# Performance work log

Measured on AMD Instinct MI355X. Metric: run time of the kernel, lower is better.

The kernel has to match this reference:

```python
import jax, jax.numpy as jnp
import numpy as np

IN_DIM = 256
HID = 384
HEADS = 6
NH1 = HID // HEADS  # 64 per-head hidden in layer1
N = 3072
SLOPE_GAT = 0.2   # LeakyReLU inside GAT attention
SLOPE_ACT = 0.01  # default nn.LeakyReLU / F.leaky_relu slope


def _leaky(x, s):
    return jnp.where(x >= 0, x, s * x)


def _gat_sublayer(h, mask, W, a, heads, nh, concat):
    # h: [N, F_in], mask: [N, N] bool, W: [heads*nh, F_in], a: [2*nh]
    n = h.shape[0]
    g = (h @ W.T).reshape(n, heads, nh)  # [N, H, F]
    # e[i,j,h] = leakyrelu(<g_i, a_l> + <g_j, a_r>)  (avoids O(N^2) concat)
    sl = jnp.einsum('nhf,f->nh', g, a[:nh])
    sr = jnp.einsum('nhf,f->nh', g, a[nh:])
    e = _leaky(sl[:, None, :] + sr[None, :, :], SLOPE_GAT)  # [N, N, H]
    e = jnp.where(mask[:, :, None], e, jnp.float32(-10000.0))
    att = jax.nn.softmax(e, axis=1)  # softmax over source nodes j
    out = jnp.einsum('ijh,jhf->ihf', att, g)
    return out.reshape(n, heads * nh) if concat else out.mean(axis=1)


def _gat(x, mask, W1, a1, W2, a2):
    x = _gat_sublayer(x, mask, W1, a1, HEADS, NH1, True)   # [N, HID]
    x = jax.nn.elu(x)
    return _gat_sublayer(x, mask, W2, a2, 1, IN_DIM, False)  # [N, IN_DIM]


def setup_inputs() -> dict:
    key = jax.random.key(0)
    ks = iter(jax.random.split(key, 32))
    d = {
        'feature': jax.random.normal(next(ks), (1, N, IN_DIM), jnp.float32),
        'adj': jax.random.randint(next(ks), (1, N, N), 0, 2, jnp.int32),
        'doc_num': 16,
        'sect_num': 192,
    }
    def w(shape, scale=0.05):
        return jax.random.normal(next(ks), shape, jnp.float32) * scale
    for br in ('sent', 'sect', 'doc'):
        d[f'W1_{br}'] = w((HID, IN_DIM))
        d[f'a1_{br}'] = w((2 * NH1,))
        d[f'W2_{br}'] = w((IN_DIM, HID))
        d[f'a2_{br}'] = w((2 * IN_DIM,))
    d['fusion_W'] = w((IN_DIM, 3 * IN_DIM)); d['fusion_b'] = jnp.zeros((IN_DIM,), jnp.float32)
    d['ffn_W0'] = w((HID, IN_DIM)); d['ffn_b0'] = jnp.zeros((HID,), jnp.float32)
    d['ffn_W1'] = w((HID, HID)); d['ffn_b1'] = jnp.zeros((HID,), jnp.float32)
    d['ffn_W2'] = w((IN_DIM, HID)); d['ffn_b2'] = jnp.zeros((IN_DIM,), jnp.float32)
    return d


def reference(feature, adj, doc_num, sect_num,
              W1_sent, a1_sent, W2_sent, a2_sent,
              W1_sect, a1_sect, W2_sect, a2_sect,
              W1_doc, a1_doc, W2_doc, a2_doc,
              fusion_W, fusion_b,
              ffn_W0, ffn_b0, ffn_W1, ffn_b1, ffn_W2, ffn_b2):
    f = feature[0]          # [N, D]
    n = f.shape[0]
    A = adj[0] != 0         # [N, N]
    cols = jnp.arange(n)
    sent_mask = A & (cols < n - sect_num - doc_num)[None, :]
    sect_mask = A & (cols >= n - sect_num - doc_num)[None, :] & (cols < n - doc_num)[None, :]
    doc_mask = A & (cols >= n - doc_num)[None, :]

    f_sent = _gat(f, sent_mask, W1_sent, a1_sent, W2_sent, a2_sent) + f
    f_sect = _gat(f, sect_mask, W1_sect, a1_sect, W2_sect, a2_sect) + f
    f_doc = _gat(f, doc_mask, W1_doc, a1_doc, W2_doc, a2_doc) + f

    fused = jnp.concatenate([f_doc, f_sect, f_sent], axis=-1)  # [N, 3D]
    fused = _leaky(fused @ fusion_W.T + fusion_b, SLOPE_ACT)
    h = _leaky(fused @ ffn_W0.T + ffn_b0, SLOPE_ACT)
    h = _leaky(h @ ffn_W1.T + ffn_b1, SLOPE_ACT)
    h = _leaky(h @ ffn_W2.T + ffn_b2, SLOPE_ACT)
    return (h + f)[None]    # [1, N, D]
```

## Files before the change

kernel.cpp:

```cpp
#include <hip/hip_runtime.h>
#include <stdint.h>

#define N_NODES 3072
#define D_IN    256
#define HIDDEN  384
#define HEADS   6
#define NH1     64
#define C1      1152
#define C2      768
#define MASK_ULL   48
#define MASK_BYTES 384
#define MASK_BSTRIDE ((size_t)N_NODES * MASK_BYTES)
#define QS      6
#define LOG2E   1.4426950408889634f

typedef __bf16 bf16;
typedef __bf16 bf16x8 __attribute__((ext_vector_type(8)));
typedef __bf16 bf16x4 __attribute__((ext_vector_type(4)));
typedef float  f32x4  __attribute__((ext_vector_type(4)));

__device__ __forceinline__ void atomAddF(float* p, float v) {
  __hip_atomic_fetch_add(p, v, __ATOMIC_RELAXED, __HIP_MEMORY_SCOPE_AGENT);
}
__device__ __forceinline__ float fexp2(float x) {
  float r; asm("v_exp_f32 %0, %1" : "=v"(r) : "v"(x)); return r;
}
__device__ __forceinline__ int bnd32(int jlo, int jhi, int len, int q, int Qb) {
  return (q >= Qb) ? ((jhi + 31) & ~31) : ((jlo + (len * q) / Qb) & ~31);
}

struct CastArgs {
  const float* src[11];
  bf16*        dst[11];
  int          cum4[12];
  int          castN;
};

__global__ __launch_bounds__(256) void prep_kernel(CastArgs A,
                                                   const int* __restrict__ adj,
                                                   unsigned long long* __restrict__ maskU,
                                                   const int* __restrict__ dnum,
                                                   const int* __restrict__ snum) {
  if ((int)blockIdx.x < A.castN) {
    int g = blockIdx.x * 256 + threadIdx.x;
    int j = 0;
#pragma unroll
    for (int k = 1; k < 11; ++k) j += (g >= A.cum4[k]);
    int e = (g - A.cum4[j]) * 4;
    float4 v = *(const float4*)(A.src[j] + e);
    bf16x4 o = { (bf16)v.x, (bf16)v.y, (bf16)v.z, (bf16)v.w };
    *(bf16x4*)(A.dst[j] + e) = o;
    return;
  }
  int dn = dnum[0], sn = snum[0];
  int bb1 = N_NODES - sn - dn, bb2 = N_NODES - dn;
  int row = blockIdx.x - A.castN;
  const int* ar = adj + (size_t)row * N_NODES;
  int lane = threadIdx.x & 63, wave = threadIdx.x >> 6;
#pragma unroll
  for (int it = 0; it < N_NODES / 256; ++it) {
    int j = it * 256 + wave * 64 + lane;
    bool a = ar[j] != 0;
    unsigned long long m0 = __ballot(a && (j < bb1));
    unsigned long long m1 = __ballot(a && (j >= bb1) && (j < bb2));
    unsigned long long m2 = __ballot(a && (j >= bb2));
    if (lane == 0) {
      size_t o = (size_t)row * MASK_ULL + it * 4 + wave;
      maskU[o] = m0;
      maskU[o + (size_t)N_NODES * MASK_ULL] = m1;
      maskU[o + 2 * (size_t)N_NODES * MASK_ULL] = m2;
    }
  }
}

template<int C>
__global__ __launch_bounds__(256) void pack_kernel(const bf16* __restrict__ src,
                                                   bf16* __restrict__ dst,
                                                   float* __restrict__ gm) {
  __shared__ bf16 t[64][72];
  int j0 = blockIdx.x * 64, f0 = blockIdx.y * 64;
  int rr = threadIdx.x >> 4;
  int cc = (threadIdx.x & 15) * 4;
#pragma unroll
  for (int p = 0; p < 4; ++p) {
    int r = p * 16 + rr;
    *(bf16x4*)&t[r][cc] = *(const bf16x4*)&src[(size_t)(j0 + r) * C + f0 + cc];
  }
  __syncthreads();
  int f = threadIdx.x & 63, g = threadIdx.x >> 6;
#pragma unroll
  for (int q = 0; q < 2; ++q) {
    int p = g * 2 + q;
    bf16x8 v = { t[p*8+0][f], t[p*8+1][f], t[p*8+2][f], t[p*8+3][f],
                 t[p*8+4][f], t[p*8+5][f], t[p*8+6][f], t[p*8+7][f] };
    *(bf16x8*)&dst[ ((size_t)((j0 >> 3) + p) * C + f0 + f) * 8 ] = v;
  }
  float s = 0.f;
#pragma unroll
  for (int k = 0; k < 16; ++k) s += (float)t[g * 16 + k][f];
  atomAddF(&gm[f0 + f], s * (1.0f / N_NODES));
}

template<int NCPB, int NH>
__global__ __launch_bounds__(256) void head_proj_kernel(
    const bf16* __restrict__ g, int ldg,
    const float* __restrict__ a0, const float* __restrict__ a1, const float* __restrict__ a2,
    float* __restrict__ elp, float* __restrict__ eln,
    float* __restrict__ erp, float* __restrict__ ern) {
  int c = blockIdx.y;
  int i = blockIdx.x * 16 + (threadIdx.x >> 4);
  int b = c / NCPB;
  const float* a = (b == 0) ? a0 : (b == 1) ? a1 : a2;
  int f0 = (threadIdx.x & 15) * (NH / 16);
  const bf16* gr = g + (size_t)i * ldg + c * NH + f0;
  float accl = 0.f, accr = 0.f;
#pragma unroll
  for (int k = 0; k < NH / 16; k += 4) {
    bf16x4 v = *(const bf16x4*)&gr[k];
#pragma unroll
    for (int e = 0; e < 4; ++e) {
      float gv = (float)v[e];
      accl += gv * a[f0 + k + e];
      accr += gv * a[NH + f0 + k + e];
    }
  }
#pragma unroll
  for (int m = 1; m < 16; m <<= 1) {
    accl += __shfl_xor(accl, m, 64);
    accr += __shfl_xor(accr, m, 64);
  }
  if ((threadIdx.x & 15) == 0) {
    int o = c * N_NODES + i;
    elp[o] = fexp2(accl * LOG2E);
    eln[o] = fexp2(0.2f * accl * LOG2E);
    erp[o] = fexp2(accr * LOG2E);
    ern[o] = fexp2(0.2f * accr * LOG2E);
  }
}

template<bool BIAS, bool LEAKY, bool RES, bool F32OUT>
__global__ __launch_bounds__(256) void gemm64_kernel(
    const bf16* __restrict__ A, int lda, int aZoff,
    const bf16* __restrict__ B0, const bf16* __restrict__ B1, const bf16* __restrict__ B2,
    int ldb, void* __restrict__ Cout, int ldc, int cZoff, int K,
    const float* __restrict__ bias, const float* __restrict__ res) {
  __shared__ bf16 As[2 * 64 * 64];
  __shared__ bf16 Bs[2 * 64 * 64];
  int z = blockIdx.z;
  const bf16* Ab = A + (size_t)z * aZoff;
  const bf16* Bb = (z == 0) ? B0 : (z == 1) ? B1 : B2;
  int m0 = blockIdx.x * 64, n0 = blockIdx.y * 64;
  int tid = threadIdx.x;
  int lane = tid & 63, wave = tid >> 6;
  int wm = wave >> 1, wn = wave & 1;
  int l15 = lane & 15, lk = lane >> 4;
  int r0 = tid >> 3, p0 = tid & 7, q0 = p0 ^ (r0 & 7);
  int r1 = (256 + tid) >> 3, p1 = tid & 7, q1 = p1 ^ (r1 & 7);
  bf16x8 ra0, ra1, rb0, rb1;
  auto gload = [&](int kt) {
    const bf16* ab = Ab + (size_t)kt * 64;
    const bf16* bb = Bb + (size_t)kt * 64;
    ra0 = *(const bf16x8*)&ab[(size_t)(m0 + r0) * lda + q0 * 8];
    ra1 = *(const bf16x8*)&ab[(size_t)(m0 + r1) * lda + q1 * 8];
    rb0 = *(const bf16x8*)&bb[(size_t)(n0 + r0) * ldb + q0 * 8];
    rb1 = *(const bf16x8*)&bb[(size_t)(n0 + r1) * ldb + q1 * 8];
  };
  auto sstore = [&](int buf) {
    bf16* as = As + buf * 4096;
    bf16* bs = Bs + buf * 4096;
    *(bf16x8*)&as[r0 * 64 + p0 * 8] = ra0;
    *(bf16x8*)&as[r1 * 64 + p1 * 8] = ra1;
    *(bf16x8*)&bs[r0 * 64 + p0 * 8] = rb0;
    *(bf16x8*)&bs[r1 * 64 + p1 * 8] = rb1;
  };
  f32x4 acc[2][2] = {};
  int nk = K >> 6;
  gload(0);
  sstore(0);
  __syncthreads();
  for (int kt = 0; kt < nk; ++kt) {
    bool more = (kt + 1) < nk;
    if (more) gload(kt + 1);
    const bf16* as = As + (kt & 1) * 4096;
    const bf16* bs = Bs + (kt & 1) * 4096;
#pragma unroll
    for (int s = 0; s < 2; ++s) {
      bf16x8 af[2], bfr[2];
      int u = s * 4 + lk;
#pragma unroll
      for (int mi = 0; mi < 2; ++mi) {
        int r = wm * 32 + mi * 16 + l15;
        af[mi] = *(const bf16x8*)&as[r * 64 + (u ^ (r & 7)) * 8];
      }
#pragma unroll
      for (int ni = 0; ni < 2; ++ni) {
        int r = wn * 32 + ni * 16 + l15;
        bfr[ni] = *(const bf16x8*)&bs[r * 64 + (u ^ (r & 7)) * 8];
      }
#pragma unroll
      for (int mi = 0; mi < 2; ++mi)
#pragma unroll
        for (int ni = 0; ni < 2; ++ni)
          acc[mi][ni] = __builtin_amdgcn_mfma_f32_16x16x32_bf16(af[mi], bfr[ni], acc[mi][ni], 0, 0, 0);
    }
    if (more) sstore((kt + 1) & 1);
    __syncthreads();
  }
#pragma unroll
  for (int mi = 0; mi < 2; ++mi)
#pragma unroll
    for (int ni = 0; ni < 2; ++ni)
#pragma unroll
      for (int r = 0; r < 4; ++r) {
        int i = m0 + wm * 32 + mi * 16 + lk * 4 + r;
        int col = z * cZoff + n0 + wn * 32 + ni * 16 + l15;
        float v = acc[mi][ni][r];
        if (BIAS) v += bias[col];
        if (LEAKY) v = (v >= 0.f) ? v : 0.01f * v;
        if (RES) v += res[(size_t)i * ldc + col];
        if (F32OUT) ((float*)Cout)[(size_t)i * ldc + col] = v;
        else        ((bf16*)Cout)[(size_t)i * ldc + col] = (bf16)v;
      }
}

struct Stream {
  float4 p0, p1, n0, n1;
  unsigned int m0, m1, m2, m3;
  bf16x8 b0, b1, b2, b3;
};

template<int C>
__device__ __forceinline__ void load_stream(
    Stream& s, int jb,
    const float* __restrict__ erpB, const float* __restrict__ ernB,
    const unsigned char* mr0, const unsigned char* mr1,
    const unsigned char* mr2, const unsigned char* mr3,
    const bf16* __restrict__ gPl) {
  s.p0 = *(const float4*)&erpB[jb];
  s.p1 = *(const float4*)&erpB[jb + 4];
  s.n0 = *(const float4*)&ernB[jb];
  s.n1 = *(const float4*)&ernB[jb + 4];
  int mo = jb >> 3;
  s.m0 = mr0[mo]; s.m1 = mr1[mo]; s.m2 = mr2[mo]; s.m3 = mr3[mo];
  const bf16* gp = gPl + (size_t)mo * C * 8;
  s.b0 = *(const bf16x8*)(gp + 0);
  s.b1 = *(const bf16x8*)(gp + 128);
  s.b2 = *(const bf16x8*)(gp + 256);
  s.b3 = *(const bf16x8*)(gp + 384);
}

template<bool L1>
__global__ __launch_bounds__(256, 2) void att_kernel(
    const bf16* __restrict__ gP,
    const float* __restrict__ elpA, const float* __restrict__ elnA,
    const float* __restrict__ erpA, const float* __restrict__ ernA,
    const unsigned char* __restrict__ maskB,
    const int* __restrict__ dnum, const int* __restrict__ snum,
    float* __restrict__ accP, float* __restrict__ lP) {
  constexpr int C = L1 ? C1 : C2;
  int c = blockIdx.y;
  int b = L1 ? (c / 6) : (c >> 2);
  int colbase = L1 ? c * 64 : (b * 256 + (c & 3) * 64);
  int sidx = L1 ? c : b;
  int q = blockIdx.z;
  int Qb = (b == 0) ? QS : 1;
  if (q >= Qb) return;
  int dn = dnum[0], sn = snum[0];
  int bb1 = N_NODES - sn - dn, bb2 = N_NODES - dn;
  int jlo = (b == 0) ? 0 : (b == 1) ? bb1 : bb2;
  int jhi = (b == 0) ? bb1 : (b == 1) ? bb2 : N_NODES;
  int len = jhi - jlo;
  int wlo = bnd32(jlo, jhi, len, q, Qb);
  int whi = bnd32(jlo, jhi, len, q + 1, Qb);
  if (wlo >= whi) return;

  int wave = threadIdx.x >> 6, lane = threadIdx.x & 63;
  int l15 = lane & 15, lk = lane >> 4;
  int row0 = blockIdx.x * 256 + wave * 64;
  float elp[4], eln[4];
  const unsigned char* mr0;
  const unsigned char* mr1;
  const unsigned char* mr2;
  const unsigned char* mr3;
  {
    const unsigned char* mbase = maskB + (size_t)b * MASK_BSTRIDE;
#pragma unroll
    for (int rg = 0; rg < 4; ++rg) {
      int ip = row0 + rg * 16 + l15;
      elp[rg] = elpA[sidx * N_NODES + ip];
      eln[rg] = elnA[sidx * N_NODES + ip];
    }
    mr0 = mbase + (size_t)(row0 + 0 * 16 + l15) * MASK_BYTES;
    mr1 = mbase + (size_t)(row0 + 1 * 16 + l15) * MASK_BYTES;
    mr2 = mbase + (size_t)(row0 + 2 * 16 + l15) * MASK_BYTES;
    mr3 = mbase + (size_t)(row0 + 3 * 16 + l15) * MASK_BYTES;
  }
  const float* erpB = erpA + sidx * N_NODES;
  const float* ernB = ernA + sidx * N_NODES;
  const bf16* gPl = gP + (size_t)(colbase + l15) * 8;
  bf16x8 ones;
#pragma unroll
  for (int e = 0; e < 8; ++e) ones[e] = (bf16)1.0f;
  f32x4 acc[4][4] = {};
  f32x4 accl[4] = {};

  auto compute = [&](const Stream& cur) {
    float pv[8] = { cur.p0.x, cur.p0.y, cur.p0.z, cur.p0.w, cur.p1.x, cur.p1.y, cur.p1.z, cur.p1.w };
    float nv[8] = { cur.n0.x, cur.n0.y, cur.n0.z, cur.n0.w, cur.n1.x, cur.n1.y, cur.n1.z, cur.n1.w };
#pragma unroll
    for (int rg = 0; rg < 4; ++rg) {
      unsigned int mb = (rg == 0) ? cur.m0 : (rg == 1) ? cur.m1 : (rg == 2) ? cur.m2 : cur.m3;
      bf16x8 a8;
#pragma unroll
      for (int e = 0; e < 8; ++e) {
        float z = elp[rg] * pv[e];
        float w = eln[rg] * nv[e];
        float p = (z >= 1.f) ? z : w;
        p = ((mb >> e) & 1u) ? p : 0.f;
        a8[e] = (bf16)p;
      }
      acc[rg][0] = __builtin_amdgcn_mfma_f32_16x16x32_bf16(a8, cur.b0, acc[rg][0], 0, 0, 0);
      acc[rg][1] = __builtin_amdgcn_mfma_f32_16x16x32_bf16(a8, cur.b1, acc[rg][1], 0, 0, 0);
      acc[rg][2] = __builtin_amdgcn_mfma_f32_16x16x32_bf16(a8, cur.b2, acc[rg][2], 0, 0, 0);
      acc[rg][3] = __builtin_amdgcn_mfma_f32_16x16x32_bf16(a8, cur.b3, acc[rg][3], 0, 0, 0);
      accl[rg] = __builtin_amdgcn_mfma_f32_16x16x32_bf16(a8, ones, accl[rg], 0, 0, 0);
    }
  };

  Stream s0, s1;
  load_stream<C>(s0, wlo + lk * 8, erpB, ernB, mr0, mr1, mr2, mr3, gPl);
  int jt = wlo;
  while (true) {
    bool m1 = (jt + 32) < whi;
    if (m1) load_stream<C>(s1, jt + 32 + lk * 8, erpB, ernB, mr0, mr1, mr2, mr3, gPl);
    compute(s0);
    if (!m1) break;
    bool m2 = (jt + 64) < whi;
    if (m2) load_stream<C>(s0, jt + 64 + lk * 8, erpB, ernB, mr0, mr1, mr2, mr3, gPl);
    compute(s1);
    if (!m2) break;
    jt += 64;
  }

  int slot = (b == 0) ? (c * QS + q) : (L1 ? (36 + (c - 6)) : (24 + (c - 4)));
  float* ap = accP + ((size_t)slot * N_NODES + row0) * 64;
#pragma unroll
  for (int rg = 0; rg < 4; ++rg)
#pragma unroll
    for (int nf = 0; nf < 4; ++nf)
#pragma unroll
      for (int r = 0; r < 4; ++r)
        ap[(rg * 16 + lk * 4 + r) * 64 + nf * 16 + l15] = acc[rg][nf][r];
  if (l15 == 0) {
#pragma unroll
    for (int rg = 0; rg < 4; ++rg)
#pragma unroll
      for (int r = 0; r < 4; ++r)
        lP[(size_t)slot * N_NODES + row0 + rg * 16 + lk * 4 + r] = accl[rg][r];
  }
}

__global__ __launch_bounds__(256) void fin1_kernel(
    const float* __restrict__ accP, const float* __restrict__ lP,
    const float* __restrict__ gm, const int* __restrict__ dnum, const int* __restrict__ snum,
    bf16* __restrict__ out1) {
  int t = blockIdx.x * 256 + threadIdx.x;
  int i = t / (C1 / 8), f0 = (t - i * (C1 / 8)) * 8;
  int c = f0 >> 6;
  int b = c / 6;
  int dn = dnum[0], sn = snum[0];
  int bb1 = N_NODES - sn - dn, bb2 = N_NODES - dn;
  int jlo = (b == 0) ? 0 : (b == 1) ? bb1 : bb2;
  int jhi = (b == 0) ? bb1 : (b == 1) ? bb2 : N_NODES;
  int len = jhi - jlo;
  int Qb = (b == 0) ? QS : 1;
  float l = 0.f;
  float a[8] = {0.f,0.f,0.f,0.f,0.f,0.f,0.f,0.f};
  if (len > 0) {
    for (int q = 0; q < Qb; ++q) {
      if (bnd32(jlo, jhi, len, q, Qb) >= bnd32(jlo, jhi, len, q + 1, Qb)) continue;
      int slot = (b == 0) ? (c * QS + q) : (36 + (c - 6));
      l += lP[(size_t)slot * N_NODES + i];
      const float* ap = &accP[((size_t)slot * N_NODES + i) * 64 + (f0 & 63)];
      f32x4 v0 = *(const f32x4*)ap, v1 = *(const f32x4*)(ap + 4);
#pragma unroll
      for (int e = 0; e < 4; ++e) { a[e] += v0[e]; a[e + 4] += v1[e]; }
    }
  }
  float inv = (l > 0.f) ? 1.f / l : 0.f;
  bf16x8 o;
#pragma unroll
  for (int e = 0; e < 8; ++e) {
    float v = (l > 0.f) ? a[e] * inv : gm[f0 + e];
    v = (v > 0.f) ? v : (__expf(v) - 1.f);
    o[e] = (bf16)v;
  }
  *(bf16x8*)&out1[(size_t)i * C1 + f0] = o;
}

__global__ __launch_bounds__(256) void fin2_kernel(
    const float* __restrict__ accP, const float* __restrict__ lP,
    const float* __restrict__ gm, const float* __restrict__ feat,
    const int* __restrict__ dnum, const int* __restrict__ snum,
    bf16* __restrict__ fused) {
  int t = blockIdx.x * 256 + threadIdx.x;
  int i = t / (C2 / 8), f0 = (t - i * (C2 / 8)) * 8;
  int b = f0 >> 8;
  int fi = f0 & 255;
  int fc = (f0 >> 6) & 3;
  int c = b * 4 + fc;
  int dn = dnum[0], sn = snum[0];
  int bb1 = N_NODES - sn - dn, bb2 = N_NODES - dn;
  int jlo = (b == 0) ? 0 : (b == 1) ? bb1 : bb2;
  int jhi = (b == 0) ? bb1 : (b == 1) ? bb2 : N_NODES;
  int len = jhi - jlo;
  int Qb = (b == 0) ? QS : 1;
  float l = 0.f;
  float a[8] = {0.f,0.f,0.f,0.f,0.f,0.f,0.f,0.f};
  if (len > 0) {
    for (int q = 0; q < Qb; ++q) {
      if (bnd32(jlo, jhi, len, q, Qb) >= bnd32(jlo, jhi, len, q + 1, Qb)) continue;
      int slot = (b == 0) ? (c * QS + q) : (24 + (c - 4));
      l += lP[(size_t)slot * N_NODES + i];
      const float* ap = &accP[((size_t)slot * N_NODES + i) * 64 + (f0 & 63)];
      f32x4 v0 = *(const f32x4*)ap, v1 = *(const f32x4*)(ap + 4);
#pragma unroll
      for (int e = 0; e < 4; ++e) { a[e] += v0[e]; a[e + 4] += v1[e]; }
    }
  }
  float inv = (l > 0.f) ? 1.f / l : 0.f;
  bf16x8 o;
#pragma unroll
  for (int e = 0; e < 8; ++e) {
    float v = (l > 0.f) ? a[e] * inv : gm[f0 + e];
    v += feat[(size_t)i * D_IN + fi + e];
    o[e] = (bf16)v;
  }
  *(bf16x8*)&fused[(size_t)i * C2 + (2 - b) * D_IN + fi] = o;
}

extern "C" void kernel_launch(void* const* d_in, const int* in_sizes, int n_in,
                              void* d_out, int out_size, void* d_ws, size_t ws_size,
                              hipStream_t stream) {
  (void)in_sizes; (void)n_in; (void)out_size; (void)ws_size;
  const float* feature = (const float*)d_in[0];
  const int*   adj     = (const int*)d_in[1];
  const int*   dnum    = (const int*)d_in[2];
  const int*   snum    = (const int*)d_in[3];
  const float* W1s = (const float*)d_in[4];  const float* a1s = (const float*)d_in[5];
  const float* W2s = (const float*)d_in[6];  const float* a2s = (const float*)d_in[7];
  const float* W1e = (const float*)d_in[8];  const float* a1e = (const float*)d_in[9];
  const float* W2e = (const float*)d_in[10]; const float* a2e = (const float*)d_in[11];
  const float* W1d = (const float*)d_in[12]; const float* a1d = (const float*)d_in[13];
  const float* W2d = (const float*)d_in[14]; const float* a2d = (const float*)d_in[15];
  const float* fW  = (const float*)d_in[16]; const float* fB  = (const float*)d_in[17];
  const float* w0  = (const float*)d_in[18]; const float* b0  = (const float*)d_in[19];
  const float* w1  = (const float*)d_in[20]; const float* b1  = (const float*)d_in[21];
  const float* w2  = (const float*)d_in[22]; const float* b2  = (const float*)d_in[23];

  char* ws = (char*)d_ws;
  size_t off = 0;
  auto alloc = [&](size_t bytes) { void* p = ws + off; off += (bytes + 255) & ~(size_t)255; return p; };

  unsigned long long* maskU = (unsigned long long*)alloc(3 * (size_t)N_NODES * MASK_ULL * 8);
  bf16* fbf   = (bf16*)alloc((size_t)N_NODES * D_IN * 2);
  bf16* w1b0  = (bf16*)alloc(HIDDEN * D_IN * 2);
  bf16* w1b1  = (bf16*)alloc(HIDDEN * D_IN * 2);
  bf16* w1b2  = (bf16*)alloc(HIDDEN * D_IN * 2);
  bf16* w2b0  = (bf16*)alloc(D_IN * HIDDEN * 2);
  bf16* w2b1  = (bf16*)alloc(D_IN * HIDDEN * 2);
  bf16* w2b2  = (bf16*)alloc(D_IN * HIDDEN * 2);
  bf16* wfusb = (bf16*)alloc(D_IN * C2 * 2);
  bf16* wf0b  = (bf16*)alloc(HIDDEN * D_IN * 2);
  bf16* wf1b  = (bf16*)alloc(HIDDEN * HIDDEN * 2);
  bf16* wf2b  = (bf16*)alloc(D_IN * HIDDEN * 2);
  bf16* g1    = (bf16*)alloc((size_t)N_NODES * C1 * 2);
  bf16* gP1   = (bf16*)alloc((size_t)N_NODES * C1 * 2);
  bf16* out1  = (bf16*)alloc((size_t)N_NODES * C1 * 2);
  bf16* g2    = (bf16*)alloc((size_t)N_NODES * C2 * 2);
  bf16* gP2   = (bf16*)alloc((size_t)N_NODES * C2 * 2);
  bf16* fusedB= (bf16*)alloc((size_t)N_NODES * C2 * 2);
  bf16* h0    = (bf16*)alloc((size_t)N_NODES * D_IN * 2);
  bf16* h1    = (bf16*)alloc((size_t)N_NODES * HIDDEN * 2);
  bf16* h2    = (bf16*)alloc((size_t)N_NODES * HIDDEN * 2);
  float* elp1 = (float*)alloc(18 * N_NODES * 4);
  float* eln1 = (float*)alloc(18 * N_NODES * 4);
  float* erp1 = (float*)alloc(18 * N_NODES * 4);
  float* ern1 = (float*)alloc(18 * N_NODES * 4);
  float* elp2 = (float*)alloc(3 * N_NODES * 4);
  float* eln2 = (float*)alloc(3 * N_NODES * 4);
  float* erp2 = (float*)alloc(3 * N_NODES * 4);
  float* ern2 = (float*)alloc(3 * N_NODES * 4);
  float* accU = (float*)alloc((size_t)48 * N_NODES * 64 * 4);
  float* lU   = (float*)alloc((size_t)48 * N_NODES * 4);
  size_t zoff = off;
  float* gm1  = (float*)alloc(C1 * 4);
  float* gm2  = (float*)alloc(C2 * 4);
  size_t zbytes = off - zoff;
  const unsigned char* maskBytes = (const unsigned char*)maskU;

  hipMemsetAsync(ws + zoff, 0, zbytes, stream);

  CastArgs ca;
  {
    const float* srcs[11] = { feature, W1s, W1e, W1d, W2s, W2e, W2d, fW, w0, w1, w2 };
    bf16* dsts[11] = { fbf, w1b0, w1b1, w1b2, w2b0, w2b1, w2b2, wfusb, wf0b, wf1b, wf2b };
    int counts[11] = { N_NODES*D_IN, HIDDEN*D_IN, HIDDEN*D_IN, HIDDEN*D_IN,
                       D_IN*HIDDEN, D_IN*HIDDEN, D_IN*HIDDEN, D_IN*C2,
                       HIDDEN*D_IN, HIDDEN*HIDDEN, D_IN*HIDDEN };
    int cum = 0;
    for (int k = 0; k < 11; ++k) { ca.src[k] = srcs[k]; ca.dst[k] = dsts[k]; ca.cum4[k] = cum; cum += counts[k] / 4; }
    ca.cum4[11] = cum;
    ca.castN = cum / 256;
    prep_kernel<<<ca.castN + N_NODES, 256, 0, stream>>>(ca, adj, maskU, dnum, snum);
  }
  gemm64_kernel<false,false,false,false><<<dim3(48,6,3), 256, 0, stream>>>(
      fbf, D_IN, 0, w1b0, w1b1, w1b2, D_IN, g1, C1, HIDDEN, D_IN, nullptr, nullptr);
  pack_kernel<C1><<<dim3(48,18), 256, 0, stream>>>(g1, gP1, gm1);
  head_proj_kernel<HEADS, NH1><<<dim3(192,18), 256, 0, stream>>>(g1, C1, a1s, a1e, a1d, elp1, eln1, erp1, ern1);
  att_kernel<true><<<dim3(12, 18, QS), 256, 0, stream>>>(gP1, elp1, eln1, erp1, ern1, maskBytes, dnum, snum, accU, lU);
  fin1_kernel<<<N_NODES * (C1 / 8) / 256, 256, 0, stream>>>(accU, lU, gm1, dnum, snum, out1);
  gemm64_kernel<false,false,false,false><<<dim3(48,4,3), 256, 0, stream>>>(
      out1, C1, HIDDEN, w2b0, w2b1, w2b2, HIDDEN, g2, C2, D_IN, HIDDEN, nullptr, nullptr);
  pack_kernel<C2><<<dim3(48,12), 256, 0, stream>>>(g2, gP2, gm2);
  head_proj_kernel<1, D_IN><<<dim3(192,3), 256, 0, stream>>>(g2, C2, a2s, a2e, a2d, elp2, eln2, erp2, ern2);
  att_kernel<false><<<dim3(12, 12, QS), 256, 0, stream>>>(gP2, elp2, eln2, erp2, ern2, maskBytes, dnum, snum, accU, lU);
  fin2_kernel<<<N_NODES * (C2 / 8) / 256, 256, 0, stream>>>(accU, lU, gm2, feature, dnum, snum, fusedB);
  gemm64_kernel<true,true,false,false><<<dim3(48,4,1), 256, 0, stream>>>(
      fusedB, C2, 0, wfusb, wfusb, wfusb, C2, h0, D_IN, 0, C2, fB, nullptr);
  gemm64_kernel<true,true,false,false><<<dim3(48,6,1), 256, 0, stream>>>(
      h0, D_IN, 0, wf0b, wf0b, wf0b, D_IN, h1, HIDDEN, 0, D_IN, b0, nullptr);
  gemm64_kernel<true,true,false,false><<<dim3(48,6,1), 256, 0, stream>>>(
      h1, HIDDEN, 0, wf1b, wf1b, wf1b, HIDDEN, h2, HIDDEN, 0, HIDDEN, b1, nullptr);
  gemm64_kernel<true,true,true,true><<<dim3(48,4,1), 256, 0, stream>>>(
      h2, HIDDEN, 0, wf2b, wf2b, wf2b, HIDDEN, d_out, D_IN, 0, HIDDEN, b2, feature);
}
```

Measured before the change: 282.3 us.

## Stage attention B-operand tiles in LDS via async global_load_lds and transpose mask

The attention kernel stops loading its packed value tiles and source scores straight into per-lane registers. It now double-buffers them into shared memory with direct global-to-LDS loads, so the four waves of a block share each tile. The adjacency bitmask is stored transposed (byte-column per node) so mask reads for consecutive rows coalesce. The cost is a block-wide barrier and full vmcnt drain every 64 columns, which may limit overlap, plus a scattered byte-write pattern in the mask prep.

```diff
diff --git a/kernel.cpp b/kernel.cpp
--- a/kernel.cpp
+++ b/kernel.cpp
@@ -9,8 +9,7 @@
 #define C1      1152
 #define C2      768
 #define MASK_ULL   48
-#define MASK_BYTES 384
-#define MASK_BSTRIDE ((size_t)N_NODES * MASK_BYTES)
+#define MT_STRIDE  ((size_t)384 * N_NODES)
 #define QS      6
 #define LOG2E   1.4426950408889634f
 
@@ -18,6 +17,16 @@
 typedef __bf16 bf16x8 __attribute__((ext_vector_type(8)));
 typedef __bf16 bf16x4 __attribute__((ext_vector_type(4)));
 typedef float  f32x4  __attribute__((ext_vector_type(4)));
+
+typedef __attribute__((address_space(1))) const unsigned int as1_u32;
+typedef __attribute__((address_space(3))) unsigned int as3_u32;
+
+__device__ __forceinline__ void gload_lds16(const void* g, void* l) {
+  __builtin_amdgcn_global_load_lds((as1_u32*)g, (as3_u32*)l, 16, 0, 0);
+}
+__device__ __forceinline__ void gload_lds4(const void* g, void* l) {
+  __builtin_amdgcn_global_load_lds((as1_u32*)g, (as3_u32*)l, 4, 0, 0);
+}
 
 __device__ __forceinline__ void atomAddF(float* p, float v) {
   __hip_atomic_fetch_add(p, v, __ATOMIC_RELAXED, __HIP_MEMORY_SCOPE_AGENT);
@@ -38,7 +47,7 @@
 
 __global__ __launch_bounds__(256) void prep_kernel(CastArgs A,
                                                    const int* __restrict__ adj,
-                                                   unsigned long long* __restrict__ maskU,
+                                                   unsigned char* __restrict__ maskT,
                                                    const int* __restrict__ dnum,
                                                    const int* __restrict__ snum) {
   if ((int)blockIdx.x < A.castN) {
@@ -64,12 +73,13 @@
     unsigned long long m0 = __ballot(a && (j < bb1));
     unsigned long long m1 = __ballot(a && (j >= bb1) && (j < bb2));
     unsigned long long m2 = __ballot(a && (j >= bb2));
-    if (lane == 0) {
-      size_t o = (size_t)row * MASK_ULL + it * 4 + wave;
-      maskU[o] = m0;
-      maskU[o + (size_t)N_NODES * MASK_ULL] = m1;
-      maskU[o + 2 * (size_t)N_NODES * MASK_ULL] = m2;
-    }
+    int moBase = it * 32 + wave * 8;
+    if (lane < 8)
+      maskT[(size_t)(moBase + lane) * N_NODES + row] = (unsigned char)(m0 >> (lane * 8));
+    else if (lane < 16)
+      maskT[MT_STRIDE + (size_t)(moBase + lane - 8) * N_NODES + row] = (unsigned char)(m1 >> ((lane - 8) * 8));
+    else if (lane < 24)
+      maskT[2 * MT_STRIDE + (size_t)(moBase + lane - 16) * N_NODES + row] = (unsigned char)(m2 >> ((lane - 16) * 8));
   }
 }
 
@@ -223,38 +233,12 @@
       }
 }
 
-struct Stream {
-  float4 p0, p1, n0, n1;
-  unsigned int m0, m1, m2, m3;
-  bf16x8 b0, b1, b2, b3;
-};
-
-template<int C>
-__device__ __forceinline__ void load_stream(
-    Stream& s, int jb,
-    const float* __restrict__ erpB, const float* __restrict__ ernB,
-    const unsigned char* mr0, const unsigned char* mr1,
-    const unsigned char* mr2, const unsigned char* mr3,
-    const bf16* __restrict__ gPl) {
-  s.p0 = *(const float4*)&erpB[jb];
-  s.p1 = *(const float4*)&erpB[jb + 4];
-  s.n0 = *(const float4*)&ernB[jb];
-  s.n1 = *(const float4*)&ernB[jb + 4];
-  int mo = jb >> 3;
-  s.m0 = mr0[mo]; s.m1 = mr1[mo]; s.m2 = mr2[mo]; s.m3 = mr3[mo];
-  const bf16* gp = gPl + (size_t)mo * C * 8;
-  s.b0 = *(const bf16x8*)(gp + 0);
-  s.b1 = *(const bf16x8*)(gp + 128);
-  s.b2 = *(const bf16x8*)(gp + 256);
-  s.b3 = *(const bf16x8*)(gp + 384);
-}
-
 template<bool L1>
 __global__ __launch_bounds__(256, 2) void att_kernel(
     const bf16* __restrict__ gP,
     const float* __restrict__ elpA, const float* __restrict__ elnA,
     const float* __restrict__ erpA, const float* __restrict__ ernA,
-    const unsigned char* __restrict__ maskB,
+    const unsigned char* __restrict__ maskT,
     const int* __restrict__ dnum, const int* __restrict__ snum,
     float* __restrict__ accP, float* __restrict__ lP) {
   constexpr int C = L1 ? C1 : C2;
@@ -274,72 +258,88 @@
   int whi = bnd32(jlo, jhi, len, q + 1, Qb);
   if (wlo >= whi) return;
 
+  __shared__ bf16  sgP[2][8][64 * 8];
+  __shared__ float serp[2][64];
+  __shared__ float sern[2][64];
+
   int wave = threadIdx.x >> 6, lane = threadIdx.x & 63;
   int l15 = lane & 15, lk = lane >> 4;
   int row0 = blockIdx.x * 256 + wave * 64;
   float elp[4], eln[4];
-  const unsigned char* mr0;
-  const unsigned char* mr1;
-  const unsigned char* mr2;
-  const unsigned char* mr3;
-  {
-    const unsigned char* mbase = maskB + (size_t)b * MASK_BSTRIDE;
-#pragma unroll
-    for (int rg = 0; rg < 4; ++rg) {
-      int ip = row0 + rg * 16 + l15;
-      elp[rg] = elpA[sidx * N_NODES + ip];
-      eln[rg] = elnA[sidx * N_NODES + ip];
-    }
-    mr0 = mbase + (size_t)(row0 + 0 * 16 + l15) * MASK_BYTES;
-    mr1 = mbase + (size_t)(row0 + 1 * 16 + l15) * MASK_BYTES;
-    mr2 = mbase + (size_t)(row0 + 2 * 16 + l15) * MASK_BYTES;
-    mr3 = mbase + (size_t)(row0 + 3 * 16 + l15) * MASK_BYTES;
+#pragma unroll
+  for (int rg = 0; rg < 4; ++rg) {
+    int ip = row0 + rg * 16 + l15;
+    elp[rg] = elpA[sidx * N_NODES + ip];
+    eln[rg] = elnA[sidx * N_NODES + ip];
   }
   const float* erpB = erpA + sidx * N_NODES;
   const float* ernB = ernA + sidx * N_NODES;
-  const bf16* gPl = gP + (size_t)(colbase + l15) * 8;
+  const bf16* gPcol = gP + (size_t)colbase * 8;
+  const unsigned char* mTb = maskT + (size_t)b * MT_STRIDE;
   bf16x8 ones;
 #pragma unroll
   for (int e = 0; e < 8; ++e) ones[e] = (bf16)1.0f;
   f32x4 acc[4][4] = {};
   f32x4 accl[4] = {};
 
-  auto compute = [&](const Stream& cur) {
-    float pv[8] = { cur.p0.x, cur.p0.y, cur.p0.z, cur.p0.w, cur.p1.x, cur.p1.y, cur.p1.z, cur.p1.w };
-    float nv[8] = { cur.n0.x, cur.n0.y, cur.n0.z, cur.n0.w, cur.n1.x, cur.n1.y, cur.n1.z, cur.n1.w };
-#pragma unroll
-    for (int rg = 0; rg < 4; ++rg) {
-      unsigned int mb = (rg == 0) ? cur.m0 : (rg == 1) ? cur.m1 : (rg == 2) ? cur.m2 : cur.m3;
-      bf16x8 a8;
-#pragma unroll
-      for (int e = 0; e < 8; ++e) {
-        float z = elp[rg] * pv[e];
-        float w = eln[rg] * nv[e];
-        float p = (z >= 1.f) ? z : w;
-        p = ((mb >> e) & 1u) ? p : 0.f;
-        a8[e] = (bf16)p;
+  auto stage = [&](int buf, int cb) {
+    int mo0 = cb >> 3;
+#pragma unroll
+    for (int k = 0; k < 2; ++k) {
+      int ml = wave * 2 + k;
+      if ((mo0 + ml) * 8 < whi)
+        gload_lds16(gPcol + ((size_t)(mo0 + ml) * C + lane) * 8, &sgP[buf][ml][0]);
+    }
+    if (wave == 0) gload_lds4(erpB + cb + lane, &serp[buf][0]);
+    if (wave == 1) gload_lds4(ernB + cb + lane, &sern[buf][0]);
+  };
+
+  int buf = 0;
+  stage(0, wlo);
+  asm volatile("s_waitcnt vmcnt(0)" ::: "memory");
+  __syncthreads();
+  for (int cb = wlo; cb < whi; cb += 64) {
+    int nb = cb + 64;
+    if (nb < whi) stage(buf ^ 1, nb);
+#pragma unroll
+    for (int h = 0; h < 2; ++h) {
+      int jt = cb + h * 32;
+      if (jt >= whi) break;
+      int lj = h * 32 + lk * 8;
+      int oct = h * 4 + lk;
+      f32x4 pv0 = *(const f32x4*)&serp[buf][lj];
+      f32x4 pv1 = *(const f32x4*)&serp[buf][lj + 4];
+      f32x4 nv0 = *(const f32x4*)&sern[buf][lj];
+      f32x4 nv1 = *(const f32x4*)&sern[buf][lj + 4];
+      bf16x8 bf0 = *(const bf16x8*)&sgP[buf][oct][(0 * 16 + l15) * 8];
+      bf16x8 bf1 = *(const bf16x8*)&sgP[buf][oct][(1 * 16 + l15) * 8];
+      bf16x8 bf2 = *(const bf16x8*)&sgP[buf][oct][(2 * 16 + l15) * 8];
+      bf16x8 bf3 = *(const bf16x8*)&sgP[buf][oct][(3 * 16 + l15) * 8];
+      const unsigned char* mT = mTb + (size_t)((jt >> 3) + lk) * N_NODES + row0;
+#pragma unroll
+      for (int rg = 0; rg < 4; ++rg) {
+        unsigned int mb = mT[rg * 16 + l15];
+        bf16x8 a8;
+#pragma unroll
+        for (int e = 0; e < 8; ++e) {
+          float pvv = (e < 4) ? pv0[e & 3] : pv1[e & 3];
+          float nvv = (e < 4) ? nv0[e & 3] : nv1[e & 3];
+          float z = elp[rg] * pvv;
+          float w = eln[rg] * nvv;
+          float p = (z >= 1.f) ? z : w;
+          p = ((mb >> e) & 1u) ? p : 0.f;
+          a8[e] = (bf16)p;
+        }
+        acc[rg][0] = __builtin_amdgcn_mfma_f32_16x16x32_bf16(a8, bf0, acc[rg][0], 0, 0, 0);
+        acc[rg][1] = __builtin_amdgcn_mfma_f32_16x16x32_bf16(a8, bf1, acc[rg][1], 0, 0, 0);
+        acc[rg][2] = __builtin_amdgcn_mfma_f32_16x16x32_bf16(a8, bf2, acc[rg][2], 0, 0, 0);
+        acc[rg][3] = __builtin_amdgcn_mfma_f32_16x16x32_bf16(a8, bf3, acc[rg][3], 0, 0, 0);
+        accl[rg]   = __builtin_amdgcn_mfma_f32_16x16x32_bf16(a8, ones, accl[rg], 0, 0, 0);
       }
-      acc[rg][0] = __builtin_amdgcn_mfma_f32_16x16x32_bf16(a8, cur.b0, acc[rg][0], 0, 0, 0);
-      acc[rg][1] = __builtin_amdgcn_mfma_f32_16x16x32_bf16(a8, cur.b1, acc[rg][1], 0, 0, 0);
-      acc[rg][2] = __builtin_amdgcn_mfma_f32_16x16x32_bf16(a8, cur.b2, acc[rg][2], 0, 0, 0);
-      acc[rg][3] = __builtin_amdgcn_mfma_f32_16x16x32_bf16(a8, cur.b3, acc[rg][3], 0, 0, 0);
-      accl[rg] = __builtin_amdgcn_mfma_f32_16x16x32_bf16(a8, ones, accl[rg], 0, 0, 0);
     }
-  };
-
-  Stream s0, s1;
-  load_stream<C>(s0, wlo + lk * 8, erpB, ernB, mr0, mr1, mr2, mr3, gPl);
-  int jt = wlo;
-  while (true) {
-    bool m1 = (jt + 32) < whi;
-    if (m1) load_stream<C>(s1, jt + 32 + lk * 8, erpB, ernB, mr0, mr1, mr2, mr3, gPl);
-    compute(s0);
-    if (!m1) break;
-    bool m2 = (jt + 64) < whi;
-    if (m2) load_stream<C>(s0, jt + 64 + lk * 8, erpB, ernB, mr0, mr1, mr2, mr3, gPl);
-    compute(s1);
-    if (!m2) break;
-    jt += 64;
+    asm volatile("s_waitcnt vmcnt(0)" ::: "memory");
+    __syncthreads();
+    buf ^= 1;
   }
 
   int slot = (b == 0) ? (c * QS + q) : (L1 ? (36 + (c - 6)) : (24 + (c - 4)));
@@ -462,7 +462,7 @@
   size_t off = 0;
   auto alloc = [&](size_t bytes) { void* p = ws + off; off += (bytes + 255) & ~(size_t)255; return p; };
 
-  unsigned long long* maskU = (unsigned long long*)alloc(3 * (size_t)N_NODES * MASK_ULL * 8);
+  unsigned char* maskT = (unsigned char*)alloc(3 * MT_STRIDE);
   bf16* fbf   = (bf16*)alloc((size_t)N_NODES * D_IN * 2);
   bf16* w1b0  = (bf16*)alloc(HIDDEN * D_IN * 2);
   bf16* w1b1  = (bf16*)alloc(HIDDEN * D_IN * 2);
@@ -497,7 +497,6 @@
   float* gm1  = (float*)alloc(C1 * 4);
   float* gm2  = (float*)alloc(C2 * 4);
   size_t zbytes = off - zoff;
-  const unsigned char* maskBytes = (const unsigned char*)maskU;
 
   hipMemsetAsync(ws + zoff, 0, zbytes, stream);
 
@@ -512,19 +511,19 @@
     for (int k = 0; k < 11; ++k) { ca.src[k] = srcs[k]; ca.dst[k] = dsts[k]; ca.cum4[k] = cum; cum += counts[k] / 4; }
     ca.cum4[11] = cum;
     ca.castN = cum / 256;
-    prep_kernel<<<ca.castN + N_NODES, 256, 0, stream>>>(ca, adj, maskU, dnum, snum);
+    prep_kernel<<<ca.castN + N_NODES, 256, 0, stream>>>(ca, adj, maskT, dnum, snum);
   }
   gemm64_kernel<false,false,false,false><<<dim3(48,6,3), 256, 0, stream>>>(
       fbf, D_IN, 0, w1b0, w1b1, w1b2, D_IN, g1, C1, HIDDEN, D_IN, nullptr, nullptr);
   pack_kernel<C1><<<dim3(48,18), 256, 0, stream>>>(g1, gP1, gm1);
   head_proj_kernel<HEADS, NH1><<<dim3(192,18), 256, 0, stream>>>(g1, C1, a1s, a1e, a1d, elp1, eln1, erp1, ern1);
-  att_kernel<true><<<dim3(12, 18, QS), 256, 0, stream>>>(gP1, elp1, eln1, erp1, ern1, maskBytes, dnum, snum, accU, lU);
+  att_kernel<true><<<dim3(12, 18, QS), 256, 0, stream>>>(gP1, elp1, eln1, erp1, ern1, maskT, dnum, snum, accU, lU);
   fin1_kernel<<<N_NODES * (C1 / 8) / 256, 256, 0, stream>>>(accU, lU, gm1, dnum, snum, out1);
   gemm64_kernel<false,false,false,false><<<dim3(48,4,3), 256, 0, stream>>>(
       out1, C1, HIDDEN, w2b0, w2b1, w2b2, HIDDEN, g2, C2, D_IN, HIDDEN, nullptr, nullptr);
   pack_kernel<C2><<<dim3(48,12), 256, 0, stream>>>(g2, gP2, gm2);
   head_proj_kernel<1, D_IN><<<dim3(192,3), 256, 0, stream>>>(g2, C2, a2s, a2e, a2d, elp2, eln2, erp2, ern2);
-  att_kernel<false><<<dim3(12, 12, QS), 256, 0, stream>>>(gP2, elp2, eln2, erp2, ern2, maskBytes, dnum, snum, accU, lU);
+  att_kernel<false><<<dim3(12, 12, QS), 256, 0, stream>>>(gP2, elp2, eln2, erp2, ern2, maskT, dnum, snum, accU, lU);
   fin2_kernel<<<N_NODES * (C2 / 8) / 256, 256, 0, stream>>>(accU, lU, gm2, feature, dnum, snum, fusedB);
   gemm64_kernel<true,true,false,false><<<dim3(48,4,1), 256, 0, stream>>>(
       fusedB, C2, 0, wfusb, wfusb, wfusb, C2, h0, D_IN, 0, C2, fB, nullptr);
```

Result: slower. 291.7 us (+3.3%).
